# Performance work log

Measured on AMD Instinct MI355X. Metric: run time of the kernel, lower is better.

The kernel has to match this reference:

```python
import jax, jax.numpy as jnp
import numpy as np

N_HEAD = 12
D_HEAD = 64  # key_dim // n_head = 768 // 12


def sparsemax(z):
    # Martins & Astudillo (2016): projection of each row of z onto the simplex.
    K = z.shape[-1]
    z_sorted = -jnp.sort(-z, axis=-1)                      # descending sort
    cs = jnp.cumsum(z_sorted, axis=-1)
    r = jnp.arange(1, K + 1, dtype=z.dtype)
    support = (1.0 + r * z_sorted) > cs                    # support set indicator
    ksz = jnp.sum(support, axis=-1, keepdims=True)         # support size k(z)
    cs_k = jnp.take_along_axis(cs, ksz.astype(jnp.int32) - 1, axis=-1)
    tau = (cs_k - 1.0) / ksz.astype(z.dtype)               # threshold
    return jnp.maximum(z - tau, 0.0)


def setup_inputs() -> dict:
    key = jax.random.key(0)
    kq, kk, kv, kwq, kbq, kwk, kbk = jax.random.split(key, 7)
    B, L, D = 8, 1024, 768
    scale = 0.02
    return {
        "q": jax.random.normal(kq, (B, L, D), jnp.float32),
        "k": jax.random.normal(kk, (B, L, D), jnp.float32),
        "v": jax.random.normal(kv, (B, L, D), jnp.float32),
        "Wq": jax.random.normal(kwq, (D, D), jnp.float32) * scale,  # torch Linear weight [out,in]
        "bq": jax.random.normal(kbq, (D,), jnp.float32) * scale,
        "Wk": jax.random.normal(kwk, (D, D), jnp.float32) * scale,
        "bk": jax.random.normal(kbk, (D,), jnp.float32) * scale,
    }


def reference(q, k, v, Wq, bq, Wk, bk):
    B, Lq, _ = q.shape
    Lkv = k.shape[1]
    # project and split heads: [B, H, L, d_head]
    qh = (q @ Wq.T + bq).reshape(B, Lq, N_HEAD, D_HEAD).transpose(0, 2, 1, 3)
    kh = (k @ Wk.T + bk).reshape(B, Lkv, N_HEAD, D_HEAD).transpose(0, 2, 1, 3)
    inv_sqrt_d = jnp.asarray(1.0 / np.sqrt(D_HEAD), q.dtype)
    scores = jnp.einsum("bhqd,bhkd->bhqk", qh, kh) * inv_sqrt_d  # [B,H,Lq,Lkv]
    attn = sparsemax(scores)
    attn = attn.mean(axis=1)                                      # head-mean -> [B,Lq,Lkv]
    # eval mode: smooth_max is identity (training-only smoothing)
    output = jnp.einsum("bqk,bkd->bqd", attn, v)                  # [B,Lq,Dv]
    return output, attn
```

## Files before the change

### kernel.cpp

```cpp
#include <hip/hip_runtime.h>

#define BSZ 8
#define NH 12
#define LSEQ 1024
#define DMODEL 768
#define DHEAD 64
#define OUT_ELEMS 6291456
#define ATTN_ELEMS 8388608

typedef __attribute__((ext_vector_type(8))) short short8;
typedef __attribute__((ext_vector_type(4))) float f32x4;

__device__ __forceinline__ int   f2i(float x) { union { float f; int i; } c; c.f = x; return c.i; }
__device__ __forceinline__ float i2f(int x)   { union { int i; float f; } c; c.i = x; return c.f; }

__device__ __forceinline__ unsigned short f2bf(float x) {
    union { float f; unsigned u; } c; c.f = x;
    unsigned r = (c.u + 0x7FFF + ((c.u >> 16) & 1)) >> 16;
    return (unsigned short)r;
}
__device__ __forceinline__ float bf2f(unsigned short h) {
    union { float f; unsigned u; } c; c.u = ((unsigned)h) << 16;
    return c.f;
}
__device__ __forceinline__ void split2(float x, unsigned short& h, unsigned short& l) {
    h = f2bf(x);
    l = f2bf(x - bf2f(h));
}

template<int CTRL>
__device__ __forceinline__ float dppadd(float v) {
    return v + i2f(__builtin_amdgcn_update_dpp(0, f2i(v), CTRL, 0xF, 0xF, true));
}
template<int CTRL>
__device__ __forceinline__ float dppmax(float v) {
    return fmaxf(v, i2f(__builtin_amdgcn_update_dpp(f2i(v), f2i(v), CTRL, 0xF, 0xF, false)));
}

__device__ __forceinline__ void wsum4(float s[4]) {
#define WS(CTRL) _Pragma("unroll") for (int rr = 0; rr < 4; ++rr) { s[rr] = dppadd<CTRL>(s[rr]); }
    WS(0x111) WS(0x112) WS(0x114) WS(0x118) WS(0x142) WS(0x143)
#undef WS
#pragma unroll
    for (int rr = 0; rr < 4; ++rr) s[rr] = i2f(__builtin_amdgcn_readlane(f2i(s[rr]), 63));
}

__device__ __forceinline__ void wsummax4(float s[4], float m[4]) {
#define WS(CTRL) _Pragma("unroll") for (int rr = 0; rr < 4; ++rr) { s[rr] = dppadd<CTRL>(s[rr]); m[rr] = dppmax<CTRL>(m[rr]); }
    WS(0x111) WS(0x112) WS(0x114) WS(0x118) WS(0x142) WS(0x143)
#undef WS
#pragma unroll
    for (int rr = 0; rr < 4; ++rr) {
        s[rr] = i2f(__builtin_amdgcn_readlane(f2i(s[rr]), 63));
        m[rr] = i2f(__builtin_amdgcn_readlane(f2i(m[rr]), 63));
    }
}

__global__ __launch_bounds__(256) void proj_mfma(
    const float* __restrict__ qin, const float* __restrict__ kin,
    const float* __restrict__ Wq, const float* __restrict__ bq,
    const float* __restrict__ Wk, const float* __restrict__ bk,
    unsigned short* __restrict__ ws) {
    const float* A; const float* W; const float* bias;
    unsigned short* hi; unsigned short* lo;
    if (blockIdx.z == 0) { A = qin; W = Wq; bias = bq; hi = ws;                lo = ws + OUT_ELEMS; }
    else                 { A = kin; W = Wk; bias = bk; hi = ws + 2*OUT_ELEMS; lo = ws + 3*OUT_ELEMS; }

    __shared__ unsigned short Ah[128][32], Al[128][32];
    __shared__ unsigned short Bh[128][32], Bl[128][32];

    const int t    = threadIdx.x;
    const int lane = t & 63;
    const int w    = t >> 6;
    const int wr   = w >> 1, wc = w & 1;
    const int mrow = lane & 15, quad = lane >> 4;
    const int m0   = blockIdx.y * 128;
    const int n0   = blockIdx.x * 128;

    const int srow = t >> 3;
    const int scol = (t & 7) * 4;

    f32x4 acc[4][4];
#pragma unroll
    for (int i = 0; i < 4; ++i)
#pragma unroll
        for (int j = 0; j < 4; ++j) acc[i][j] = (f32x4){0.f, 0.f, 0.f, 0.f};

    for (int k0 = 0; k0 < DMODEL; k0 += 32) {
        float4 av[4], wv[4];
#pragma unroll
        for (int i = 0; i < 4; ++i) {
            av[i] = *(const float4*)&A[(size_t)(m0 + srow + i * 32) * DMODEL + k0 + scol];
            wv[i] = *(const float4*)&W[(size_t)(n0 + srow + i * 32) * DMODEL + k0 + scol];
        }
        __syncthreads();
#pragma unroll
        for (int i = 0; i < 4; ++i) {
            ushort4 h4, l4;
            split2(av[i].x, h4.x, l4.x); split2(av[i].y, h4.y, l4.y);
            split2(av[i].z, h4.z, l4.z); split2(av[i].w, h4.w, l4.w);
            *(ushort4*)&Ah[srow + i * 32][scol] = h4;
            *(ushort4*)&Al[srow + i * 32][scol] = l4;
            split2(wv[i].x, h4.x, l4.x); split2(wv[i].y, h4.y, l4.y);
            split2(wv[i].z, h4.z, l4.z); split2(wv[i].w, h4.w, l4.w);
            *(ushort4*)&Bh[srow + i * 32][scol] = h4;
            *(ushort4*)&Bl[srow + i * 32][scol] = l4;
        }
        __syncthreads();

        short8 ah[4], al[4], bh[4], bl[4];
#pragma unroll
        for (int i = 0; i < 4; ++i) {
            ah[i] = *(const short8*)&Ah[wr * 64 + i * 16 + mrow][quad * 8];
            al[i] = *(const short8*)&Al[wr * 64 + i * 16 + mrow][quad * 8];
            bh[i] = *(const short8*)&Bh[wc * 64 + i * 16 + mrow][quad * 8];
            bl[i] = *(const short8*)&Bl[wc * 64 + i * 16 + mrow][quad * 8];
        }
#pragma unroll
        for (int i = 0; i < 4; ++i)
#pragma unroll
            for (int j = 0; j < 4; ++j) {
                acc[i][j] = __builtin_amdgcn_mfma_f32_16x16x32_bf16(al[i], bh[j], acc[i][j], 0, 0, 0);
                acc[i][j] = __builtin_amdgcn_mfma_f32_16x16x32_bf16(ah[i], bl[j], acc[i][j], 0, 0, 0);
                acc[i][j] = __builtin_amdgcn_mfma_f32_16x16x32_bf16(ah[i], bh[j], acc[i][j], 0, 0, 0);
            }
    }

#pragma unroll
    for (int j = 0; j < 4; ++j) {
        const int ng = n0 + wc * 64 + j * 16 + mrow;
        const float bj = bias[ng];
        const int hh = ng >> 6, dd = ng & 63;
#pragma unroll
        for (int i = 0; i < 4; ++i) {
#pragma unroll
            for (int reg = 0; reg < 4; ++reg) {
                const int mg = m0 + wr * 64 + i * 16 + quad * 4 + reg;
                const float c = acc[i][j][reg] + bj;
                unsigned short ch, cl;
                split2(c, ch, cl);
                const size_t idx = (((size_t)(mg >> 10) * NH + hh) * LSEQ + (mg & 1023)) * DHEAD + dd;
                hi[idx] = ch;
                lo[idx] = cl;
            }
        }
    }
}

__global__ __launch_bounds__(256, 2) void attn_kernel(
    const unsigned short* __restrict__ ws, float* __restrict__ attn_out) {
    __shared__ float S[16 * 1024];

    const unsigned short* Qhi = ws;
    const unsigned short* Qlo = ws + OUT_ELEMS;
    const unsigned short* Khi = ws + 2 * OUT_ELEMS;
    const unsigned short* Klo = ws + 3 * OUT_ELEMS;

    const int t = threadIdx.x;
    const int lane = t & 63;
    const int w = t >> 6;
    const int b = blockIdx.y;
    const int q0 = blockIdx.x * 16;

    const int mrow = lane & 15;
    const int quad = lane >> 4;

    f32x4 acc[16];
#pragma unroll
    for (int j = 0; j < 16; ++j) acc[j] = (f32x4){0.f, 0.f, 0.f, 0.f};

    for (int h = 0; h < NH; ++h) {
        const size_t hb = ((size_t)b * NH + h) * (LSEQ * DHEAD);

        const size_t aoff = hb + (size_t)(q0 + mrow) * DHEAD + quad * 8;
        short8 ah0 = *(const short8*)(Qhi + aoff);
        short8 ah1 = *(const short8*)(Qhi + aoff + 32);
        short8 al0 = *(const short8*)(Qlo + aoff);
        short8 al1 = *(const short8*)(Qlo + aoff + 32);

        __syncthreads();

#pragma unroll 4
        for (int nt = 0; nt < 16; ++nt) {
            const int n0 = w * 256 + nt * 16;
            const size_t boff = hb + (size_t)(n0 + mrow) * DHEAD + quad * 8;
            short8 bh0 = *(const short8*)(Khi + boff);
            short8 bh1 = *(const short8*)(Khi + boff + 32);
            short8 bl0 = *(const short8*)(Klo + boff);
            short8 bl1 = *(const short8*)(Klo + boff + 32);
            f32x4 d = {0.f, 0.f, 0.f, 0.f};
            d = __builtin_amdgcn_mfma_f32_16x16x32_bf16(al0, bh0, d, 0, 0, 0);
            d = __builtin_amdgcn_mfma_f32_16x16x32_bf16(ah0, bl0, d, 0, 0, 0);
            d = __builtin_amdgcn_mfma_f32_16x16x32_bf16(ah0, bh0, d, 0, 0, 0);
            d = __builtin_amdgcn_mfma_f32_16x16x32_bf16(al1, bh1, d, 0, 0, 0);
            d = __builtin_amdgcn_mfma_f32_16x16x32_bf16(ah1, bl1, d, 0, 0, 0);
            d = __builtin_amdgcn_mfma_f32_16x16x32_bf16(ah1, bh1, d, 0, 0, 0);
#pragma unroll
            for (int reg = 0; reg < 4; ++reg)
                S[(quad * 4 + reg) * 1024 + n0 + mrow] = d[reg] * 0.125f;
        }
        __syncthreads();

        {
            float z[4][16];
            float sv[4], mv[4];
#pragma unroll
            for (int rr = 0; rr < 4; ++rr) {
                const int r = w * 4 + rr;
#pragma unroll
                for (int c = 0; c < 4; ++c)
                    *(f32x4*)&z[rr][c * 4] = *(const f32x4*)&S[r * 1024 + c * 256 + lane * 4];
                float s = 0.f, m = z[rr][0];
#pragma unroll
                for (int j = 0; j < 16; ++j) s += z[rr][j];
#pragma unroll
                for (int j = 1; j < 16; ++j) m = fmaxf(m, z[rr][j]);
                sv[rr] = s; mv[rr] = m;
            }
            wsummax4(sv, mv);

            float tau[4]; int prev[4]; bool done[4];
#pragma unroll
            for (int rr = 0; rr < 4; ++rr) {
                tau[rr] = fmaxf((sv[rr] - 1.0f) * (1.0f / 1024.0f), mv[rr] - 1.0f);
                prev[rr] = -1; done[rr] = false;
            }

            for (int it = 0; it < 64; ++it) {
                float s4[4]; int c4[4];
#pragma unroll
                for (int rr = 0; rr < 4; ++rr) {
                    float s = 0.f; int c = 0;
#pragma unroll
                    for (int j = 0; j < 16; ++j) {
                        bool gt = z[rr][j] > tau[rr];
                        c += __popcll(__ballot(gt));
                        s += gt ? z[rr][j] : 0.f;
                    }
                    s4[rr] = s; c4[rr] = c;
                }
                wsum4(s4);
                bool alldone = true;
#pragma unroll
                for (int rr = 0; rr < 4; ++rr) {
                    if (!done[rr]) {
                        if (c4[rr] == prev[rr]) done[rr] = true;
                        else { tau[rr] = (s4[rr] - 1.0f) / (float)c4[rr]; prev[rr] = c4[rr]; }
                    }
                    alldone = alldone && done[rr];
                }
                if (alldone) break;
            }

#pragma unroll
            for (int rr = 0; rr < 4; ++rr) {
                const int r = w * 4 + rr;
#pragma unroll
                for (int c = 0; c < 4; ++c) {
                    f32x4 p;
#pragma unroll
                    for (int j = 0; j < 4; ++j)
                        p[j] = fmaxf(z[rr][c * 4 + j] - tau[rr], 0.f);
                    *(f32x4*)&S[r * 1024 + c * 256 + lane * 4] = p;
                }
            }
        }
        __syncthreads();

#pragma unroll
        for (int j = 0; j < 16; ++j) {
            f32x4 vv = *(const f32x4*)&S[j * 1024 + t * 4];
            acc[j] += vv;
        }
    }

    float* ao = attn_out + ((size_t)b * LSEQ + q0) * LSEQ;
#pragma unroll
    for (int j = 0; j < 16; ++j) {
        f32x4 o = acc[j] * (1.0f / 12.0f);
        *(f32x4*)&ao[(size_t)j * LSEQ + t * 4] = o;
    }
}

__global__ __launch_bounds__(256) void out_mfma(
    const float* __restrict__ attn, const float* __restrict__ v,
    float* __restrict__ out) {
    const int b = blockIdx.z;
    const float* Ab = attn + (size_t)b * LSEQ * LSEQ;
    const float* Vb = v    + (size_t)b * LSEQ * DMODEL;
    float* Cb       = out  + (size_t)b * LSEQ * DMODEL;

    __shared__ unsigned short Ah[128][32], Al[128][32];
    __shared__ unsigned short Bh[128][36], Bl[128][36];

    const int t    = threadIdx.x;
    const int lane = t & 63;
    const int w    = t >> 6;
    const int wr   = w >> 1, wc = w & 1;
    const int mrow = lane & 15, quad = lane >> 4;
    const int m0   = blockIdx.y * 128;
    const int n0   = blockIdx.x * 128;

    const int srow = t >> 3;
    const int scol = (t & 7) * 4;
    const int bn   = t & 127;
    const int bk0  = (t >> 7) * 16;

    f32x4 acc[4][4];
#pragma unroll
    for (int i = 0; i < 4; ++i)
#pragma unroll
        for (int j = 0; j < 4; ++j) acc[i][j] = (f32x4){0.f, 0.f, 0.f, 0.f};

    for (int k0 = 0; k0 < LSEQ; k0 += 32) {
        float4 av[4];
#pragma unroll
        for (int i = 0; i < 4; ++i)
            av[i] = *(const float4*)&Ab[(size_t)(m0 + srow + i * 32) * LSEQ + k0 + scol];
        float bv[16];
#pragma unroll
        for (int i = 0; i < 16; ++i)
            bv[i] = Vb[(size_t)(k0 + bk0 + i) * DMODEL + n0 + bn];

        __syncthreads();
#pragma unroll
        for (int i = 0; i < 4; ++i) {
            ushort4 h4, l4;
            split2(av[i].x, h4.x, l4.x); split2(av[i].y, h4.y, l4.y);
            split2(av[i].z, h4.z, l4.z); split2(av[i].w, h4.w, l4.w);
            *(ushort4*)&Ah[srow + i * 32][scol] = h4;
            *(ushort4*)&Al[srow + i * 32][scol] = l4;
        }
#pragma unroll
        for (int g = 0; g < 4; ++g) {
            ushort4 h4, l4;
            split2(bv[g * 4 + 0], h4.x, l4.x); split2(bv[g * 4 + 1], h4.y, l4.y);
            split2(bv[g * 4 + 2], h4.z, l4.z); split2(bv[g * 4 + 3], h4.w, l4.w);
            *(ushort4*)&Bh[bn][bk0 + g * 4] = h4;
            *(ushort4*)&Bl[bn][bk0 + g * 4] = l4;
        }
        __syncthreads();

        short8 ah[4], al[4], bh[4], bl[4];
#pragma unroll
        for (int i = 0; i < 4; ++i) {
            ah[i] = *(const short8*)&Ah[wr * 64 + i * 16 + mrow][quad * 8];
            al[i] = *(const short8*)&Al[wr * 64 + i * 16 + mrow][quad * 8];
        }
#pragma unroll
        for (int j = 0; j < 4; ++j) {
            const unsigned short* ph = &Bh[wc * 64 + j * 16 + mrow][quad * 8];
            const unsigned short* pl = &Bl[wc * 64 + j * 16 + mrow][quad * 8];
            uint2 h0 = *(const uint2*)ph;
            uint2 h1 = *(const uint2*)(ph + 4);
            uint2 l0 = *(const uint2*)pl;
            uint2 l1 = *(const uint2*)(pl + 4);
            union { uint u[4]; short8 s; } ch, cl;
            ch.u[0] = h0.x; ch.u[1] = h0.y; ch.u[2] = h1.x; ch.u[3] = h1.y;
            cl.u[0] = l0.x; cl.u[1] = l0.y; cl.u[2] = l1.x; cl.u[3] = l1.y;
            bh[j] = ch.s; bl[j] = cl.s;
        }
#pragma unroll
        for (int i = 0; i < 4; ++i)
#pragma unroll
            for (int j = 0; j < 4; ++j) {
                acc[i][j] = __builtin_amdgcn_mfma_f32_16x16x32_bf16(al[i], bh[j], acc[i][j], 0, 0, 0);
                acc[i][j] = __builtin_amdgcn_mfma_f32_16x16x32_bf16(ah[i], bl[j], acc[i][j], 0, 0, 0);
                acc[i][j] = __builtin_amdgcn_mfma_f32_16x16x32_bf16(ah[i], bh[j], acc[i][j], 0, 0, 0);
            }
    }

#pragma unroll
    for (int i = 0; i < 4; ++i)
#pragma unroll
        for (int j = 0; j < 4; ++j)
#pragma unroll
            for (int reg = 0; reg < 4; ++reg) {
                const int mg = m0 + wr * 64 + i * 16 + quad * 4 + reg;
                const int ng = n0 + wc * 64 + j * 16 + mrow;
                Cb[(size_t)mg * DMODEL + ng] = acc[i][j][reg];
            }
}

extern "C" void kernel_launch(void* const* d_in, const int* in_sizes, int n_in,
                              void* d_out, int out_size, void* d_ws, size_t ws_size,
                              hipStream_t stream) {
    const float* q  = (const float*)d_in[0];
    const float* k  = (const float*)d_in[1];
    const float* v  = (const float*)d_in[2];
    const float* Wq = (const float*)d_in[3];
    const float* bq = (const float*)d_in[4];
    const float* Wk = (const float*)d_in[5];
    const float* bk = (const float*)d_in[6];

    float* out  = (float*)d_out;
    float* attn = out + OUT_ELEMS;
    unsigned short* ws = (unsigned short*)d_ws;

    hipLaunchKernelGGL(proj_mfma, dim3(6, 64, 2), dim3(256), 0, stream,
                       q, k, Wq, bq, Wk, bk, ws);
    hipLaunchKernelGGL(attn_kernel, dim3(64, 8), dim3(256), 0, stream,
                       ws, attn);
    hipLaunchKernelGGL(out_mfma, dim3(6, 8, 8), dim3(256), 0, stream,
                       attn, v, out);
}
```

Measured before the change: 554.0 us.

## Use 512-thread attention blocks with row-owned head-mean accumulation and swizzled LDS

The attention kernel now runs 8 waves per block instead of 4. Each wave computes 128 score columns and owns 2 rows for the sparsemax threshold search instead of 4. The head-mean accumulator lives in registers tied to the rows each wave owns. This removes the write-back of probabilities to LDS, one barrier per head, and the strided LDS re-read. An XOR swizzle on score columns reduces LDS bank conflicts, and the sum, max and ballot reductions are split into independent chains for ILP. The trade-off is more waves contending on barriers and a 4-blocks-per-CU launch bound, which may constrain registers.

```diff
diff --git a/kernel.cpp b/kernel.cpp
--- a/kernel.cpp
+++ b/kernel.cpp
@@ -37,20 +37,20 @@
     return fmaxf(v, i2f(__builtin_amdgcn_update_dpp(f2i(v), f2i(v), CTRL, 0xF, 0xF, false)));
 }
 
-__device__ __forceinline__ void wsum4(float s[4]) {
-#define WS(CTRL) _Pragma("unroll") for (int rr = 0; rr < 4; ++rr) { s[rr] = dppadd<CTRL>(s[rr]); }
+__device__ __forceinline__ void wsum2(float s[2]) {
+#define WS(CTRL) _Pragma("unroll") for (int rr = 0; rr < 2; ++rr) { s[rr] = dppadd<CTRL>(s[rr]); }
     WS(0x111) WS(0x112) WS(0x114) WS(0x118) WS(0x142) WS(0x143)
 #undef WS
 #pragma unroll
-    for (int rr = 0; rr < 4; ++rr) s[rr] = i2f(__builtin_amdgcn_readlane(f2i(s[rr]), 63));
-}
-
-__device__ __forceinline__ void wsummax4(float s[4], float m[4]) {
-#define WS(CTRL) _Pragma("unroll") for (int rr = 0; rr < 4; ++rr) { s[rr] = dppadd<CTRL>(s[rr]); m[rr] = dppmax<CTRL>(m[rr]); }
+    for (int rr = 0; rr < 2; ++rr) s[rr] = i2f(__builtin_amdgcn_readlane(f2i(s[rr]), 63));
+}
+
+__device__ __forceinline__ void wsummax2(float s[2], float m[2]) {
+#define WS(CTRL) _Pragma("unroll") for (int rr = 0; rr < 2; ++rr) { s[rr] = dppadd<CTRL>(s[rr]); m[rr] = dppmax<CTRL>(m[rr]); }
     WS(0x111) WS(0x112) WS(0x114) WS(0x118) WS(0x142) WS(0x143)
 #undef WS
 #pragma unroll
-    for (int rr = 0; rr < 4; ++rr) {
+    for (int rr = 0; rr < 2; ++rr) {
         s[rr] = i2f(__builtin_amdgcn_readlane(f2i(s[rr]), 63));
         m[rr] = i2f(__builtin_amdgcn_readlane(f2i(m[rr]), 63));
     }
@@ -147,7 +147,7 @@
     }
 }
 
-__global__ __launch_bounds__(256, 2) void attn_kernel(
+__global__ __launch_bounds__(512, 4) void attn_kernel(
     const unsigned short* __restrict__ ws, float* __restrict__ attn_out) {
     __shared__ float S[16 * 1024];
 
@@ -165,9 +165,11 @@
     const int mrow = lane & 15;
     const int quad = lane >> 4;
 
-    f32x4 acc[16];
-#pragma unroll
-    for (int j = 0; j < 16; ++j) acc[j] = (f32x4){0.f, 0.f, 0.f, 0.f};
+    float macc[2][16];
+#pragma unroll
+    for (int rr = 0; rr < 2; ++rr)
+#pragma unroll
+        for (int j = 0; j < 16; ++j) macc[rr][j] = 0.f;
 
     for (int h = 0; h < NH; ++h) {
         const size_t hb = ((size_t)b * NH + h) * (LSEQ * DHEAD);
@@ -180,9 +182,9 @@
 
         __syncthreads();
 
-#pragma unroll 4
-        for (int nt = 0; nt < 16; ++nt) {
-            const int n0 = w * 256 + nt * 16;
+#pragma unroll 2
+        for (int nt = 0; nt < 8; ++nt) {
+            const int n0 = w * 128 + nt * 16;
             const size_t boff = hb + (size_t)(n0 + mrow) * DHEAD + quad * 8;
             short8 bh0 = *(const short8*)(Khi + boff);
             short8 bh1 = *(const short8*)(Khi + boff + 32);
@@ -195,90 +197,98 @@
             d = __builtin_amdgcn_mfma_f32_16x16x32_bf16(al1, bh1, d, 0, 0, 0);
             d = __builtin_amdgcn_mfma_f32_16x16x32_bf16(ah1, bl1, d, 0, 0, 0);
             d = __builtin_amdgcn_mfma_f32_16x16x32_bf16(ah1, bh1, d, 0, 0, 0);
+            const int swcol = (n0 + mrow) ^ (quad << 4);
 #pragma unroll
             for (int reg = 0; reg < 4; ++reg)
-                S[(quad * 4 + reg) * 1024 + n0 + mrow] = d[reg] * 0.125f;
-        }
-        __syncthreads();
-
-        {
-            float z[4][16];
-            float sv[4], mv[4];
-#pragma unroll
-            for (int rr = 0; rr < 4; ++rr) {
-                const int r = w * 4 + rr;
-#pragma unroll
-                for (int c = 0; c < 4; ++c)
-                    *(f32x4*)&z[rr][c * 4] = *(const f32x4*)&S[r * 1024 + c * 256 + lane * 4];
-                float s = 0.f, m = z[rr][0];
-#pragma unroll
-                for (int j = 0; j < 16; ++j) s += z[rr][j];
-#pragma unroll
-                for (int j = 1; j < 16; ++j) m = fmaxf(m, z[rr][j]);
-                sv[rr] = s; mv[rr] = m;
-            }
-            wsummax4(sv, mv);
-
-            float tau[4]; int prev[4]; bool done[4];
-#pragma unroll
-            for (int rr = 0; rr < 4; ++rr) {
-                tau[rr] = fmaxf((sv[rr] - 1.0f) * (1.0f / 1024.0f), mv[rr] - 1.0f);
-                prev[rr] = -1; done[rr] = false;
-            }
-
-            for (int it = 0; it < 64; ++it) {
-                float s4[4]; int c4[4];
-#pragma unroll
-                for (int rr = 0; rr < 4; ++rr) {
-                    float s = 0.f; int c = 0;
-#pragma unroll
-                    for (int j = 0; j < 16; ++j) {
-                        bool gt = z[rr][j] > tau[rr];
-                        c += __popcll(__ballot(gt));
-                        s += gt ? z[rr][j] : 0.f;
-                    }
-                    s4[rr] = s; c4[rr] = c;
+                S[(quad * 4 + reg) * 1024 + swcol] = d[reg] * 0.125f;
+        }
+        __syncthreads();
+
+        float z[2][16];
+        float sv[2], mv[2];
+#pragma unroll
+        for (int rr = 0; rr < 2; ++rr) {
+            const int r = w * 2 + rr;
+            const int swz = (r >> 2) << 4;
+#pragma unroll
+            for (int c = 0; c < 4; ++c)
+                *(f32x4*)&z[rr][c * 4] = *(const f32x4*)&S[r * 1024 + ((c * 256 + lane * 4) ^ swz)];
+            float s0 = 0.f, s1 = 0.f, s2 = 0.f, s3 = 0.f;
+            float m0 = z[rr][0], m1 = z[rr][1], m2 = z[rr][2], m3 = z[rr][3];
+#pragma unroll
+            for (int j = 0; j < 16; j += 4) {
+                s0 += z[rr][j]; s1 += z[rr][j + 1]; s2 += z[rr][j + 2]; s3 += z[rr][j + 3];
+            }
+#pragma unroll
+            for (int j = 4; j < 16; j += 4) {
+                m0 = fmaxf(m0, z[rr][j]);     m1 = fmaxf(m1, z[rr][j + 1]);
+                m2 = fmaxf(m2, z[rr][j + 2]); m3 = fmaxf(m3, z[rr][j + 3]);
+            }
+            sv[rr] = (s0 + s1) + (s2 + s3);
+            mv[rr] = fmaxf(fmaxf(m0, m1), fmaxf(m2, m3));
+        }
+        wsummax2(sv, mv);
+
+        float tau[2]; int prev[2]; bool done[2];
+#pragma unroll
+        for (int rr = 0; rr < 2; ++rr) {
+            tau[rr] = fmaxf((sv[rr] - 1.0f) * (1.0f / 1024.0f), mv[rr] - 1.0f);
+            prev[rr] = -1; done[rr] = false;
+        }
+
+        for (int it = 0; it < 64; ++it) {
+            float sI[2]; int cI[2];
+#pragma unroll
+            for (int rr = 0; rr < 2; ++rr) {
+                float a0 = 0.f, a1 = 0.f, a2 = 0.f, a3 = 0.f;
+                int c = 0;
+#pragma unroll
+                for (int j = 0; j < 16; j += 4) {
+                    bool g0 = z[rr][j]     > tau[rr];
+                    bool g1 = z[rr][j + 1] > tau[rr];
+                    bool g2 = z[rr][j + 2] > tau[rr];
+                    bool g3 = z[rr][j + 3] > tau[rr];
+                    c += __popcll(__ballot(g0)) + __popcll(__ballot(g1))
+                       + __popcll(__ballot(g2)) + __popcll(__ballot(g3));
+                    a0 += g0 ? z[rr][j]     : 0.f;
+                    a1 += g1 ? z[rr][j + 1] : 0.f;
+                    a2 += g2 ? z[rr][j + 2] : 0.f;
+                    a3 += g3 ? z[rr][j + 3] : 0.f;
                 }
-                wsum4(s4);
-                bool alldone = true;
-#pragma unroll
-                for (int rr = 0; rr < 4; ++rr) {
-                    if (!done[rr]) {
-                        if (c4[rr] == prev[rr]) done[rr] = true;
-                        else { tau[rr] = (s4[rr] - 1.0f) / (float)c4[rr]; prev[rr] = c4[rr]; }
-                    }
-                    alldone = alldone && done[rr];
+                sI[rr] = (a0 + a1) + (a2 + a3);
+                cI[rr] = c;
+            }
+            wsum2(sI);
+            bool alldone = true;
+#pragma unroll
+            for (int rr = 0; rr < 2; ++rr) {
+                if (!done[rr]) {
+                    if (cI[rr] == prev[rr]) done[rr] = true;
+                    else { tau[rr] = (sI[rr] - 1.0f) / (float)cI[rr]; prev[rr] = cI[rr]; }
                 }
-                if (alldone) break;
-            }
-
-#pragma unroll
-            for (int rr = 0; rr < 4; ++rr) {
-                const int r = w * 4 + rr;
-#pragma unroll
-                for (int c = 0; c < 4; ++c) {
-                    f32x4 p;
-#pragma unroll
-                    for (int j = 0; j < 4; ++j)
-                        p[j] = fmaxf(z[rr][c * 4 + j] - tau[rr], 0.f);
-                    *(f32x4*)&S[r * 1024 + c * 256 + lane * 4] = p;
-                }
-            }
-        }
-        __syncthreads();
-
-#pragma unroll
-        for (int j = 0; j < 16; ++j) {
-            f32x4 vv = *(const f32x4*)&S[j * 1024 + t * 4];
-            acc[j] += vv;
-        }
+                alldone = alldone && done[rr];
+            }
+            if (alldone) break;
+        }
+
+#pragma unroll
+        for (int rr = 0; rr < 2; ++rr)
+#pragma unroll
+            for (int j = 0; j < 16; ++j)
+                macc[rr][j] += fmaxf(z[rr][j] - tau[rr], 0.f);
     }
 
     float* ao = attn_out + ((size_t)b * LSEQ + q0) * LSEQ;
 #pragma unroll
-    for (int j = 0; j < 16; ++j) {
-        f32x4 o = acc[j] * (1.0f / 12.0f);
-        *(f32x4*)&ao[(size_t)j * LSEQ + t * 4] = o;
+    for (int rr = 0; rr < 2; ++rr) {
+        const int r = w * 2 + rr;
+#pragma unroll
+        for (int c = 0; c < 4; ++c) {
+            f32x4 o;
+#pragma unroll
+            for (int j = 0; j < 4; ++j) o[j] = macc[rr][c * 4 + j] * (1.0f / 12.0f);
+            *(f32x4*)&ao[(size_t)r * LSEQ + c * 256 + lane * 4] = o;
+        }
     }
 }
 
@@ -399,7 +409,7 @@
 
     hipLaunchKernelGGL(proj_mfma, dim3(6, 64, 2), dim3(256), 0, stream,
                        q, k, Wq, bq, Wk, bk, ws);
-    hipLaunchKernelGGL(attn_kernel, dim3(64, 8), dim3(256), 0, stream,
+    hipLaunchKernelGGL(attn_kernel, dim3(64, 8), dim3(512), 0, stream,
                        ws, attn);
     hipLaunchKernelGGL(out_mfma, dim3(6, 8, 8), dim3(256), 0, stream,
                        attn, v, out);
```

Measured after the change: 511.7 us. 7.6% less time.
